# Kernel tuning notes

Measured on AMD Instinct MI355X. Metric: run time of the kernel, lower is better.

The kernel has to match this reference:

```python
import jax, jax.numpy as jnp
import numpy as np

N_NODES = 100000
N_EDGES = 3200000
F_IN = 256
D_OUT = 64
BATCH = 4096
N_FIELDS = 20


def setup_inputs() -> dict:
    key = jax.random.key(0)
    k1, k2, k3, k4 = jax.random.split(key, 4)
    features = jax.random.normal(k1, (N_NODES, F_IN), dtype=jnp.float32)
    edge_index = jax.random.randint(k2, (2, N_EDGES), 0, N_NODES, dtype=jnp.int32)
    W = jax.random.normal(k3, (F_IN, D_OUT), dtype=jnp.float32) * 0.05
    b = jnp.zeros((D_OUT,), dtype=jnp.float32)
    x = jax.random.randint(k4, (BATCH, N_FIELDS), 0, N_NODES, dtype=jnp.int32)
    return {"features": features, "edge_index": edge_index, "W": W, "b": b, "x": x}


def reference(features, edge_index, W, b, x):
    # PyG GCNConv: add self-loops, symmetric normalization, linear transform,
    # scatter-add aggregation, then final index by x.
    n = features.shape[0]
    loop = jnp.arange(n, dtype=edge_index.dtype)
    src = jnp.concatenate([edge_index[0], loop])  # [E+N]
    dst = jnp.concatenate([edge_index[1], loop])
    ones = jnp.ones(src.shape[0], dtype=features.dtype)
    deg = jax.ops.segment_sum(ones, dst, num_segments=n)  # in-degree incl. self-loop
    deg_inv_sqrt = jnp.where(deg > 0, jax.lax.rsqrt(deg), 0.0)
    norm = deg_inv_sqrt[src] * deg_inv_sqrt[dst]  # [E+N]
    xw = features @ W  # [N, D] -- transform before aggregation (fewer FLOPs)
    msg = xw[src] * norm[:, None]  # gather + scale
    out = jax.ops.segment_sum(msg, dst, num_segments=n) + b  # [N, D]
    return out[x]  # [batch, num_fields, D]
```

## Files before the change

### kernel.cpp

```cpp
#include <hip/hip_runtime.h>
#include <hip/hip_bf16.h>

#define N_NODES 100000
#define N_EDGES 3200000
#define F_IN 256
#define D_OUT 64
#define BATCH 4096
#define N_FIELDS 20
#define N_ENTRIES (BATCH * N_FIELDS)

#define NBUCKET 512
#define NPB 196
#define N_PAD (NBUCKET * NPB)
#define EPB 4096
#define NBLK ((N_EDGES + EPB - 1) / EPB)
#define BUCKET_CAP 8192
#define SCAN_B 512
#define NSB (N_PAD / SCAN_B)
#define CNT_BLKS (N_ENTRIES / 256)
#define GEMM_BLKS ((N_NODES + 63) / 64)

typedef short bf16x8 __attribute__((ext_vector_type(8)));
typedef float f32x4 __attribute__((ext_vector_type(4)));

static __device__ __forceinline__ unsigned short f2bf_bits(float x) {
    __hip_bfloat16 h = __float2bfloat16(x);
    return *reinterpret_cast<unsigned short*>(&h);
}

__global__ __launch_bounds__(256) void k_front(const uint4* __restrict__ dst4,
                                               unsigned short* __restrict__ perBlockCnt,
                                               const int* __restrict__ x,
                                               int* __restrict__ nodeEntCnt,
                                               unsigned* __restrict__ refBits,
                                               const float* __restrict__ feat,
                                               const float* __restrict__ W,
                                               float* __restrict__ yf) {
    __shared__ unsigned hist[NBUCKET];
    __shared__ unsigned short wt[64 * 264];
    int tid = threadIdx.x;

    if (blockIdx.x < NBLK) {
        hist[tid] = 0;
        hist[tid + 256] = 0;
        __syncthreads();
        int base4 = blockIdx.x * (EPB / 4);
#pragma unroll
        for (int k = 0; k < EPB / 1024; k++) {
            int e4 = base4 + k * 256 + tid;
            if (e4 < N_EDGES / 4) {
                uint4 d = dst4[e4];
                atomicAdd(&hist[d.x / NPB], 1u);
                atomicAdd(&hist[d.y / NPB], 1u);
                atomicAdd(&hist[d.z / NPB], 1u);
                atomicAdd(&hist[d.w / NPB], 1u);
            }
        }
        __syncthreads();
        perBlockCnt[(tid) * NBLK + blockIdx.x] = (unsigned short)hist[tid];
        perBlockCnt[(tid + 256) * NBLK + blockIdx.x] = (unsigned short)hist[tid + 256];
    } else if (blockIdx.x < NBLK + CNT_BLKS) {
        int ent = (blockIdx.x - NBLK) * 256 + tid;
        if (ent < N_ENTRIES) {
            int node = x[ent];
            atomicAdd(&nodeEntCnt[node], 1);
            atomicOr(&refBits[node >> 5], 1u << (node & 31));
        }
    } else {
        int gb = blockIdx.x - NBLK - CNT_BLKS;
        {
            const float4* wrow = (const float4*)(W + tid * 64);
#pragma unroll
            for (int n4 = 0; n4 < 16; n4++) {
                float4 v = wrow[n4];
                wt[(n4 * 4 + 0) * 264 + tid] = f2bf_bits(v.x);
                wt[(n4 * 4 + 1) * 264 + tid] = f2bf_bits(v.y);
                wt[(n4 * 4 + 2) * 264 + tid] = f2bf_bits(v.z);
                wt[(n4 * 4 + 3) * 264 + tid] = f2bf_bits(v.w);
            }
        }
        __syncthreads();

        int wave = tid >> 6, lane = tid & 63;
        int quad = lane >> 4, m = lane & 15;
        int rowT = gb * 64 + wave * 16;
        int row = rowT + m;
        int rowC = (row < N_NODES) ? row : (N_NODES - 1);
        const float* fb = feat + (size_t)rowC * F_IN + quad * 8;

        f32x4 acc0 = {0.f, 0.f, 0.f, 0.f};
        f32x4 acc1 = acc0, acc2 = acc0, acc3 = acc0;

#pragma unroll
        for (int kk = 0; kk < 8; kk++) {
            float4 x0 = *(const float4*)(fb + kk * 32);
            float4 x1 = *(const float4*)(fb + kk * 32 + 4);
            bf16x8 a;
            a[0] = (short)f2bf_bits(x0.x); a[1] = (short)f2bf_bits(x0.y);
            a[2] = (short)f2bf_bits(x0.z); a[3] = (short)f2bf_bits(x0.w);
            a[4] = (short)f2bf_bits(x1.x); a[5] = (short)f2bf_bits(x1.y);
            a[6] = (short)f2bf_bits(x1.z); a[7] = (short)f2bf_bits(x1.w);
            int kbase = kk * 32 + quad * 8;
            bf16x8 b0 = *(const bf16x8*)&wt[(0 * 16 + m) * 264 + kbase];
            bf16x8 b1 = *(const bf16x8*)&wt[(1 * 16 + m) * 264 + kbase];
            bf16x8 b2 = *(const bf16x8*)&wt[(2 * 16 + m) * 264 + kbase];
            bf16x8 b3 = *(const bf16x8*)&wt[(3 * 16 + m) * 264 + kbase];
            acc0 = __builtin_amdgcn_mfma_f32_16x16x32_bf16(a, b0, acc0, 0, 0, 0);
            acc1 = __builtin_amdgcn_mfma_f32_16x16x32_bf16(a, b1, acc1, 0, 0, 0);
            acc2 = __builtin_amdgcn_mfma_f32_16x16x32_bf16(a, b2, acc2, 0, 0, 0);
            acc3 = __builtin_amdgcn_mfma_f32_16x16x32_bf16(a, b3, acc3, 0, 0, 0);
        }

#pragma unroll
        for (int r = 0; r < 4; r++) {
            int rr = rowT + quad * 4 + r;
            if (rr < N_NODES) {
                size_t o = (size_t)rr * D_OUT + m;
                yf[o]      = acc0[r];
                yf[o + 16] = acc1[r];
                yf[o + 32] = acc2[r];
                yf[o + 48] = acc3[r];
            }
        }
    }
}

__global__ __launch_bounds__(512) void k_scans(const int* __restrict__ nodeEntCnt,
                                               int* __restrict__ localE,
                                               int* __restrict__ blockSumsE,
                                               unsigned short* __restrict__ perBlockCnt,
                                               int* __restrict__ bucketTot) {
    if (blockIdx.x < NSB) {
        __shared__ int sh[SCAN_B];
        int g = blockIdx.x * SCAN_B + threadIdx.x;
        int v = (g < N_PAD) ? nodeEntCnt[g] : 0;
        sh[threadIdx.x] = v;
        __syncthreads();
        for (int off = 1; off < SCAN_B; off <<= 1) {
            int t = (threadIdx.x >= off) ? sh[threadIdx.x - off] : 0;
            __syncthreads();
            sh[threadIdx.x] += t;
            __syncthreads();
        }
        int incl = sh[threadIdx.x];
        if (g < N_PAD) localE[g] = incl - v;
        if (threadIdx.x == SCAN_B - 1) blockSumsE[blockIdx.x] = incl;
    } else {
        int gw = ((blockIdx.x - NSB) * 512 + threadIdx.x) >> 6;
        int lane = threadIdx.x & 63;
        if (gw >= NBUCKET) return;
        unsigned running = 0;
        for (int c = 0; c < (NBLK + 63) / 64; c++) {
            int blk = c * 64 + lane;
            int idx = gw * NBLK + blk;
            unsigned v = (blk < NBLK) ? perBlockCnt[idx] : 0;
            unsigned orig = v;
#pragma unroll
            for (int d = 1; d < 64; d <<= 1) {
                unsigned t = __shfl_up(v, d, 64);
                if (lane >= d) v += t;
            }
            if (blk < NBLK) perBlockCnt[idx] = (unsigned short)(running + v - orig);
            running += __shfl(v, 63, 64);
        }
        if (lane == 0) bucketTot[gw] = (int)running;
    }
}

__global__ __launch_bounds__(512) void k_base2(const int* __restrict__ bucketTot,
                                               int* __restrict__ bucketBase,
                                               const int* __restrict__ blockSumsE,
                                               int* __restrict__ blockBaseE) {
    __shared__ int sh[512];
    int tid = threadIdx.x;
    if (blockIdx.x == 0) {
        int v = bucketTot[tid];
        sh[tid] = v;
        __syncthreads();
        for (int off = 1; off < 512; off <<= 1) {
            int t = (tid >= off) ? sh[tid - off] : 0;
            __syncthreads();
            sh[tid] += t;
            __syncthreads();
        }
        bucketBase[tid] = sh[tid] - v;
        if (tid == NBUCKET - 1) bucketBase[NBUCKET] = sh[NBUCKET - 1];
    } else {
        int v = (tid < NSB) ? blockSumsE[tid] : 0;
        sh[tid] = v;
        __syncthreads();
        for (int off = 1; off < 512; off <<= 1) {
            int t = (tid >= off) ? sh[tid - off] : 0;
            __syncthreads();
            sh[tid] += t;
            __syncthreads();
        }
        if (tid < NSB) blockBaseE[tid] = sh[tid] - v;
    }
}

__global__ __launch_bounds__(256) void k_scatters(const uint4* __restrict__ src4,
                                                  const uint4* __restrict__ dst4,
                                                  const int* __restrict__ bucketBase,
                                                  const unsigned short* __restrict__ perBlockCnt,
                                                  unsigned* __restrict__ bucketData,
                                                  const int* __restrict__ x,
                                                  int* __restrict__ localE,
                                                  const int* __restrict__ blockBaseE,
                                                  int* __restrict__ entGrouped) {
    if (blockIdx.x < NBLK) {
        __shared__ unsigned slotBase[NBUCKET];
        slotBase[threadIdx.x] = (unsigned)bucketBase[threadIdx.x] +
                                (unsigned)perBlockCnt[threadIdx.x * NBLK + blockIdx.x];
        slotBase[threadIdx.x + 256] = (unsigned)bucketBase[threadIdx.x + 256] +
                                      (unsigned)perBlockCnt[(threadIdx.x + 256) * NBLK + blockIdx.x];
        __syncthreads();
        int base4 = blockIdx.x * (EPB / 4);
#pragma unroll
        for (int k = 0; k < EPB / 1024; k++) {
            int e4 = base4 + k * 256 + threadIdx.x;
            if (e4 < N_EDGES / 4) {
                uint4 s = src4[e4];
                uint4 d = dst4[e4];
                unsigned ss[4] = {s.x, s.y, s.z, s.w};
                unsigned dd[4] = {d.x, d.y, d.z, d.w};
#pragma unroll
                for (int j = 0; j < 4; j++) {
                    unsigned b = dd[j] / NPB;
                    unsigned ld = dd[j] - b * NPB;
                    unsigned slot = atomicAdd(&slotBase[b], 1u);
                    bucketData[slot] = ss[j] | (ld << 17);
                }
            }
        }
    } else {
        int ent = (blockIdx.x - NBLK) * 256 + threadIdx.x;
        if (ent < N_ENTRIES) {
            int node = x[ent];
            int posL = atomicAdd(&localE[node], 1);
            entGrouped[blockBaseE[node >> 9] + posL] = ent;
        }
    }
}

__global__ __launch_bounds__(256) void k_bucket_csr(unsigned* __restrict__ bucketData,
                                                    const int* __restrict__ bucketBase,
                                                    const unsigned* __restrict__ refBits,
                                                    int* __restrict__ rowStart,
                                                    unsigned short* __restrict__ deg,
                                                    const float* __restrict__ yf,
                                                    unsigned short* __restrict__ y) {
    __shared__ unsigned srcsorted[BUCKET_CAP];
    __shared__ unsigned nodeCount[NPB];
    __shared__ unsigned sscan[256];
    __shared__ unsigned cursor[NPB];
    __shared__ unsigned char refF[NPB];

    int b = blockIdx.x;
    int base = bucketBase[b];
    int cnt = bucketBase[b + 1] - base;
    if (cnt > BUCKET_CAP) cnt = BUCKET_CAP;
    int tid = threadIdx.x;

    for (int j = tid; j < NPB; j += 256) nodeCount[j] = 0;
    __syncthreads();

    for (int i = tid; i < cnt; i += 256) {
        unsigned w = bucketData[base + i];
        atomicAdd(&nodeCount[w >> 17], 1u);
    }
    __syncthreads();

    int firstNode = b * NPB;
    unsigned refCnt = 0;
    if (tid < NPB) {
        int node = firstNode + tid;
        unsigned isRef = (refBits[node >> 5] >> (node & 31)) & 1u;
        refF[tid] = (unsigned char)isRef;
        refCnt = isRef ? nodeCount[tid] : 0;
        deg[node] = (unsigned short)nodeCount[tid];
    }
    sscan[tid] = refCnt;
    __syncthreads();
    for (int off = 1; off < 256; off <<= 1) {
        unsigned t = (tid >= off) ? sscan[tid - off] : 0;
        __syncthreads();
        sscan[tid] += t;
        __syncthreads();
    }

    if (tid < NPB) {
        unsigned excl = sscan[tid] - refCnt;
        rowStart[firstNode + tid] = base + (int)excl;
        cursor[tid] = excl;
    }
    __syncthreads();

    for (int i = tid; i < cnt; i += 256) {
        unsigned w = bucketData[base + i];
        unsigned ld = w >> 17;
        if (refF[ld]) {
            unsigned slot = atomicAdd(&cursor[ld], 1u);
            srcsorted[slot] = w & 0x1FFFFu;
        }
    }
    __syncthreads();

    int refTotal = (int)sscan[255];
    for (int i = tid; i < refTotal; i += 256)
        bucketData[base + i] = srcsorted[i];

    for (int idx = tid; idx < NPB * 16; idx += 256) {
        int j = idx >> 4;
        int node = firstNode + j;
        if (node < N_NODES) {
            float ds = rsqrtf((float)nodeCount[j] + 1.0f);
            float4 v = ((const float4*)(yf + (size_t)node * D_OUT))[idx & 15];
            uint2 pw;
            pw.x = (unsigned)f2bf_bits(v.x * ds) | ((unsigned)f2bf_bits(v.y * ds) << 16);
            pw.y = (unsigned)f2bf_bits(v.z * ds) | ((unsigned)f2bf_bits(v.w * ds) << 16);
            ((uint2*)(y + (size_t)node * D_OUT))[idx & 15] = pw;
        }
    }
}

static __device__ __forceinline__ void acc4(f32x4& a, uint2 v, float msk) {
    a[0] += msk * __uint_as_float(v.x << 16);
    a[1] += msk * __uint_as_float(v.x & 0xffff0000u);
    a[2] += msk * __uint_as_float(v.y << 16);
    a[3] += msk * __uint_as_float(v.y & 0xffff0000u);
}

__global__ __launch_bounds__(256) void k_agg(const int* __restrict__ entGrouped,
                                             const int* __restrict__ localE,
                                             const int* __restrict__ blockBaseE,
                                             const int* __restrict__ rowStart,
                                             const unsigned short* __restrict__ deg,
                                             const unsigned* __restrict__ sortedSrc,
                                             const unsigned short* __restrict__ y,
                                             const float* __restrict__ b,
                                             float* __restrict__ out) {
    int g = blockIdx.x * blockDim.x + threadIdx.x;
    int i = g >> 6, lane = g & 63;
    if (i >= N_PAD) return;
    int gEnd = blockBaseE[i >> 9] + localE[i];
    int gStart = (i == 0) ? 0 : (blockBaseE[(i - 1) >> 9] + localE[i - 1]);
    int cntEnt = gEnd - gStart;
    if (cntEnt <= 0) return;

    int grp = lane >> 4;
    int m = lane & 15;
    int start = rowStart[i];
    int cnt = deg[i];
    float disI = rsqrtf((float)(cnt + 1));

    uint2 sv = *(const uint2*)(y + ((unsigned)i << 6) + (m << 2));

    f32x4 a0 = {0.f, 0.f, 0.f, 0.f};
    f32x4 a1 = a0, a2 = a0, a3 = a0;

    for (int e = 0; e < cnt; e += 32) {
        int e0 = e + grp,      e1 = e + 4 + grp,  e2 = e + 8 + grp,  e3 = e + 12 + grp;
        int e4 = e + 16 + grp, e5 = e + 20 + grp, e6 = e + 24 + grp, e7 = e + 28 + grp;
        unsigned r0 = (e0 < cnt) ? sortedSrc[start + e0] : (unsigned)i;
        unsigned r1 = (e1 < cnt) ? sortedSrc[start + e1] : (unsigned)i;
        unsigned r2 = (e2 < cnt) ? sortedSrc[start + e2] : (unsigned)i;
        unsigned r3 = (e3 < cnt) ? sortedSrc[start + e3] : (unsigned)i;
        unsigned r4 = (e4 < cnt) ? sortedSrc[start + e4] : (unsigned)i;
        unsigned r5 = (e5 < cnt) ? sortedSrc[start + e5] : (unsigned)i;
        unsigned r6 = (e6 < cnt) ? sortedSrc[start + e6] : (unsigned)i;
        unsigned r7 = (e7 < cnt) ? sortedSrc[start + e7] : (unsigned)i;
        uint2 v0 = *(const uint2*)(y + (r0 << 6) + (m << 2));
        uint2 v1 = *(const uint2*)(y + (r1 << 6) + (m << 2));
        uint2 v2 = *(const uint2*)(y + (r2 << 6) + (m << 2));
        uint2 v3 = *(const uint2*)(y + (r3 << 6) + (m << 2));
        uint2 v4 = *(const uint2*)(y + (r4 << 6) + (m << 2));
        uint2 v5 = *(const uint2*)(y + (r5 << 6) + (m << 2));
        uint2 v6 = *(const uint2*)(y + (r6 << 6) + (m << 2));
        uint2 v7 = *(const uint2*)(y + (r7 << 6) + (m << 2));
        acc4(a0, v0, (e0 < cnt) ? 1.f : 0.f);
        acc4(a1, v1, (e1 < cnt) ? 1.f : 0.f);
        acc4(a2, v2, (e2 < cnt) ? 1.f : 0.f);
        acc4(a3, v3, (e3 < cnt) ? 1.f : 0.f);
        acc4(a0, v4, (e4 < cnt) ? 1.f : 0.f);
        acc4(a1, v5, (e5 < cnt) ? 1.f : 0.f);
        acc4(a2, v6, (e6 < cnt) ? 1.f : 0.f);
        acc4(a3, v7, (e7 < cnt) ? 1.f : 0.f);
    }

    f32x4 s;
#pragma unroll
    for (int c = 0; c < 4; c++) s[c] = (a0[c] + a1[c]) + (a2[c] + a3[c]);
#pragma unroll
    for (int c = 0; c < 4; c++) {
        s[c] += __shfl_xor(s[c], 16, 64);
        s[c] += __shfl_xor(s[c], 32, 64);
    }

    float4 b4 = *(const float4*)(b + (m << 2));
    float4 val;
    val.x = disI * (s[0] + __uint_as_float(sv.x << 16)) + b4.x;
    val.y = disI * (s[1] + __uint_as_float(sv.x & 0xffff0000u)) + b4.y;
    val.z = disI * (s[2] + __uint_as_float(sv.y << 16)) + b4.z;
    val.w = disI * (s[3] + __uint_as_float(sv.y & 0xffff0000u)) + b4.w;

    for (int j = grp; j < cntEnt; j += 4) {
        int ent = entGrouped[gStart + j];
        *(float4*)(out + (size_t)ent * D_OUT + (m << 2)) = val;
    }
}

extern "C" void kernel_launch(void* const* d_in, const int* in_sizes, int n_in,
                              void* d_out, int out_size, void* d_ws, size_t ws_size,
                              hipStream_t stream) {
    const float* feat     = (const float*)d_in[0];
    const int* edge_index = (const int*)d_in[1];
    const float* W        = (const float*)d_in[2];
    const float* bsrc     = (const float*)d_in[3];
    const int* x          = (const int*)d_in[4];
    float* out            = (float*)d_out;

    const uint4* src4 = (const uint4*)edge_index;
    const uint4* dst4 = (const uint4*)(edge_index + N_EDGES);

    char* ws = (char*)d_ws;
    size_t off = 0;
    auto alloc = [&](size_t bytes) {
        size_t o = off;
        off = (off + bytes + 255) & ~(size_t)255;
        return o;
    };
    size_t pcBytes = (size_t)NBUCKET * NBLK * 2;
    size_t rsBytes = (pcBytes > (size_t)N_PAD * 4) ? pcBytes : (size_t)N_PAD * 4;
    int* bucketBase = (int*)(ws + alloc((size_t)(NBUCKET + 1) * 4));
    int* bucketTot  = (int*)(ws + alloc((size_t)NBUCKET * 4));
    size_t ecOff = alloc((size_t)N_PAD * 4);
    int* nodeEntCnt = (int*)(ws + ecOff);
    int* entGrouped = (int*)(ws + ecOff);
    unsigned* refBits = (unsigned*)(ws + alloc((size_t)(N_PAD / 8)));
    size_t rsOff = alloc(rsBytes);
    unsigned short* perBlockCnt = (unsigned short*)(ws + rsOff);
    int* rowStart   = (int*)(ws + rsOff);
    unsigned short* deg = (unsigned short*)(ws + alloc((size_t)N_PAD * 2));
    int* localE     = (int*)(ws + alloc((size_t)N_PAD * 4));
    int* blockSumsE = (int*)(ws + alloc((size_t)NSB * 4));
    int* blockBaseE = (int*)(ws + alloc((size_t)NSB * 4));
    unsigned* bucketData = (unsigned*)(ws + alloc((size_t)N_EDGES * 4));
    unsigned short* y = (unsigned short*)(ws + alloc((size_t)N_NODES * D_OUT * 2));
    float* yf       = (float*)(ws + alloc((size_t)N_NODES * D_OUT * 4));
    (void)ws_size; (void)in_sizes; (void)n_in; (void)out_size;

    const int T = 256;
    (void)hipMemsetAsync(nodeEntCnt, 0, (size_t)N_PAD * 4, stream);
    (void)hipMemsetAsync(refBits, 0, (size_t)(N_PAD / 8), stream);
    k_front<<<NBLK + CNT_BLKS + GEMM_BLKS, T, 0, stream>>>(dst4, perBlockCnt, x, nodeEntCnt,
                                                           refBits, feat, W, yf);
    k_scans<<<NSB + 64, 512, 0, stream>>>(nodeEntCnt, localE, blockSumsE, perBlockCnt, bucketTot);
    k_base2<<<2, 512, 0, stream>>>(bucketTot, bucketBase, blockSumsE, blockBaseE);
    k_scatters<<<NBLK + CNT_BLKS, T, 0, stream>>>(src4, dst4, bucketBase, perBlockCnt, bucketData,
                                                  x, localE, blockBaseE, entGrouped);
    k_bucket_csr<<<NBUCKET, T, 0, stream>>>(bucketData, bucketBase, refBits, rowStart, deg, yf, y);
    k_agg<<<((size_t)N_PAD * 64 + T - 1) / T, T, 0, stream>>>(
        entGrouped, localE, blockBaseE, rowStart, deg, bucketData, y, bsrc, out);
}
```

Baseline: 314.5 us.

## Replace scan-based bucket partition with atomic cursors and broadcast per-node results

The edge bucketing now reserves space per bucket with global atomic cursors into fixed-capacity bucket regions, all inside the front kernel. This removes the per-block histogram scans, the base-offset kernel and the separate scatter pass. The entry grouping by node is also dropped: aggregation writes per-node results for referenced nodes to a buffer, and a new broadcast kernel gathers those rows into the output by x. This cuts three launches and several passes over the data, in exchange for nondeterministic edge order within a bucket, silent truncation if a bucket exceeds its capacity, and an extra intermediate write and read.

```diff
diff --git a/kernel.cpp b/kernel.cpp
--- a/kernel.cpp
+++ b/kernel.cpp
@@ -15,10 +15,9 @@
 #define EPB 4096
 #define NBLK ((N_EDGES + EPB - 1) / EPB)
 #define BUCKET_CAP 8192
-#define SCAN_B 512
-#define NSB (N_PAD / SCAN_B)
 #define CNT_BLKS (N_ENTRIES / 256)
 #define GEMM_BLKS ((N_NODES + 63) / 64)
+#define BCAST_BLKS (N_ENTRIES / 16)
 
 typedef short bf16x8 __attribute__((ext_vector_type(8)));
 typedef float f32x4 __attribute__((ext_vector_type(4)));
@@ -28,21 +27,22 @@
     return *reinterpret_cast<unsigned short*>(&h);
 }
 
-__global__ __launch_bounds__(256) void k_front(const uint4* __restrict__ dst4,
-                                               unsigned short* __restrict__ perBlockCnt,
+__global__ __launch_bounds__(256) void k_front(const uint4* __restrict__ src4,
+                                               const uint4* __restrict__ dst4,
+                                               unsigned* __restrict__ gCursor,
+                                               unsigned* __restrict__ bucketData,
                                                const int* __restrict__ x,
-                                               int* __restrict__ nodeEntCnt,
                                                unsigned* __restrict__ refBits,
                                                const float* __restrict__ feat,
                                                const float* __restrict__ W,
                                                float* __restrict__ yf) {
-    __shared__ unsigned hist[NBUCKET];
+    __shared__ unsigned cur[NBUCKET];
     __shared__ unsigned short wt[64 * 264];
     int tid = threadIdx.x;
 
     if (blockIdx.x < NBLK) {
-        hist[tid] = 0;
-        hist[tid + 256] = 0;
+        cur[tid] = 0;
+        cur[tid + 256] = 0;
         __syncthreads();
         int base4 = blockIdx.x * (EPB / 4);
 #pragma unroll
@@ -50,20 +50,42 @@
             int e4 = base4 + k * 256 + tid;
             if (e4 < N_EDGES / 4) {
                 uint4 d = dst4[e4];
-                atomicAdd(&hist[d.x / NPB], 1u);
-                atomicAdd(&hist[d.y / NPB], 1u);
-                atomicAdd(&hist[d.z / NPB], 1u);
-                atomicAdd(&hist[d.w / NPB], 1u);
+                atomicAdd(&cur[d.x / NPB], 1u);
+                atomicAdd(&cur[d.y / NPB], 1u);
+                atomicAdd(&cur[d.z / NPB], 1u);
+                atomicAdd(&cur[d.w / NPB], 1u);
             }
         }
         __syncthreads();
-        perBlockCnt[(tid) * NBLK + blockIdx.x] = (unsigned short)hist[tid];
-        perBlockCnt[(tid + 256) * NBLK + blockIdx.x] = (unsigned short)hist[tid + 256];
+        unsigned c0 = cur[tid], c1 = cur[tid + 256];
+        unsigned b0 = c0 ? atomicAdd(&gCursor[tid], c0) : 0u;
+        unsigned b1 = c1 ? atomicAdd(&gCursor[tid + 256], c1) : 0u;
+        __syncthreads();
+        cur[tid] = (unsigned)tid * BUCKET_CAP + b0;
+        cur[tid + 256] = (unsigned)(tid + 256) * BUCKET_CAP + b1;
+        __syncthreads();
+#pragma unroll
+        for (int k = 0; k < EPB / 1024; k++) {
+            int e4 = base4 + k * 256 + tid;
+            if (e4 < N_EDGES / 4) {
+                uint4 s = src4[e4];
+                uint4 d = dst4[e4];
+                unsigned ss[4] = {s.x, s.y, s.z, s.w};
+                unsigned dd[4] = {d.x, d.y, d.z, d.w};
+#pragma unroll
+                for (int j = 0; j < 4; j++) {
+                    unsigned b = dd[j] / NPB;
+                    unsigned ld = dd[j] - b * NPB;
+                    unsigned slot = atomicAdd(&cur[b], 1u);
+                    if (slot < (b + 1u) * BUCKET_CAP)
+                        bucketData[slot] = ss[j] | (ld << 17);
+                }
+            }
+        }
     } else if (blockIdx.x < NBLK + CNT_BLKS) {
         int ent = (blockIdx.x - NBLK) * 256 + tid;
         if (ent < N_ENTRIES) {
             int node = x[ent];
-            atomicAdd(&nodeEntCnt[node], 1);
             atomicOr(&refBits[node >> 5], 1u << (node & 31));
         }
     } else {
@@ -125,126 +147,8 @@
     }
 }
 
-__global__ __launch_bounds__(512) void k_scans(const int* __restrict__ nodeEntCnt,
-                                               int* __restrict__ localE,
-                                               int* __restrict__ blockSumsE,
-                                               unsigned short* __restrict__ perBlockCnt,
-                                               int* __restrict__ bucketTot) {
-    if (blockIdx.x < NSB) {
-        __shared__ int sh[SCAN_B];
-        int g = blockIdx.x * SCAN_B + threadIdx.x;
-        int v = (g < N_PAD) ? nodeEntCnt[g] : 0;
-        sh[threadIdx.x] = v;
-        __syncthreads();
-        for (int off = 1; off < SCAN_B; off <<= 1) {
-            int t = (threadIdx.x >= off) ? sh[threadIdx.x - off] : 0;
-            __syncthreads();
-            sh[threadIdx.x] += t;
-            __syncthreads();
-        }
-        int incl = sh[threadIdx.x];
-        if (g < N_PAD) localE[g] = incl - v;
-        if (threadIdx.x == SCAN_B - 1) blockSumsE[blockIdx.x] = incl;
-    } else {
-        int gw = ((blockIdx.x - NSB) * 512 + threadIdx.x) >> 6;
-        int lane = threadIdx.x & 63;
-        if (gw >= NBUCKET) return;
-        unsigned running = 0;
-        for (int c = 0; c < (NBLK + 63) / 64; c++) {
-            int blk = c * 64 + lane;
-            int idx = gw * NBLK + blk;
-            unsigned v = (blk < NBLK) ? perBlockCnt[idx] : 0;
-            unsigned orig = v;
-#pragma unroll
-            for (int d = 1; d < 64; d <<= 1) {
-                unsigned t = __shfl_up(v, d, 64);
-                if (lane >= d) v += t;
-            }
-            if (blk < NBLK) perBlockCnt[idx] = (unsigned short)(running + v - orig);
-            running += __shfl(v, 63, 64);
-        }
-        if (lane == 0) bucketTot[gw] = (int)running;
-    }
-}
-
-__global__ __launch_bounds__(512) void k_base2(const int* __restrict__ bucketTot,
-                                               int* __restrict__ bucketBase,
-                                               const int* __restrict__ blockSumsE,
-                                               int* __restrict__ blockBaseE) {
-    __shared__ int sh[512];
-    int tid = threadIdx.x;
-    if (blockIdx.x == 0) {
-        int v = bucketTot[tid];
-        sh[tid] = v;
-        __syncthreads();
-        for (int off = 1; off < 512; off <<= 1) {
-            int t = (tid >= off) ? sh[tid - off] : 0;
-            __syncthreads();
-            sh[tid] += t;
-            __syncthreads();
-        }
-        bucketBase[tid] = sh[tid] - v;
-        if (tid == NBUCKET - 1) bucketBase[NBUCKET] = sh[NBUCKET - 1];
-    } else {
-        int v = (tid < NSB) ? blockSumsE[tid] : 0;
-        sh[tid] = v;
-        __syncthreads();
-        for (int off = 1; off < 512; off <<= 1) {
-            int t = (tid >= off) ? sh[tid - off] : 0;
-            __syncthreads();
-            sh[tid] += t;
-            __syncthreads();
-        }
-        if (tid < NSB) blockBaseE[tid] = sh[tid] - v;
-    }
-}
-
-__global__ __launch_bounds__(256) void k_scatters(const uint4* __restrict__ src4,
-                                                  const uint4* __restrict__ dst4,
-                                                  const int* __restrict__ bucketBase,
-                                                  const unsigned short* __restrict__ perBlockCnt,
-                                                  unsigned* __restrict__ bucketData,
-                                                  const int* __restrict__ x,
-                                                  int* __restrict__ localE,
-                                                  const int* __restrict__ blockBaseE,
-                                                  int* __restrict__ entGrouped) {
-    if (blockIdx.x < NBLK) {
-        __shared__ unsigned slotBase[NBUCKET];
-        slotBase[threadIdx.x] = (unsigned)bucketBase[threadIdx.x] +
-                                (unsigned)perBlockCnt[threadIdx.x * NBLK + blockIdx.x];
-        slotBase[threadIdx.x + 256] = (unsigned)bucketBase[threadIdx.x + 256] +
-                                      (unsigned)perBlockCnt[(threadIdx.x + 256) * NBLK + blockIdx.x];
-        __syncthreads();
-        int base4 = blockIdx.x * (EPB / 4);
-#pragma unroll
-        for (int k = 0; k < EPB / 1024; k++) {
-            int e4 = base4 + k * 256 + threadIdx.x;
-            if (e4 < N_EDGES / 4) {
-                uint4 s = src4[e4];
-                uint4 d = dst4[e4];
-                unsigned ss[4] = {s.x, s.y, s.z, s.w};
-                unsigned dd[4] = {d.x, d.y, d.z, d.w};
-#pragma unroll
-                for (int j = 0; j < 4; j++) {
-                    unsigned b = dd[j] / NPB;
-                    unsigned ld = dd[j] - b * NPB;
-                    unsigned slot = atomicAdd(&slotBase[b], 1u);
-                    bucketData[slot] = ss[j] | (ld << 17);
-                }
-            }
-        }
-    } else {
-        int ent = (blockIdx.x - NBLK) * 256 + threadIdx.x;
-        if (ent < N_ENTRIES) {
-            int node = x[ent];
-            int posL = atomicAdd(&localE[node], 1);
-            entGrouped[blockBaseE[node >> 9] + posL] = ent;
-        }
-    }
-}
-
 __global__ __launch_bounds__(256) void k_bucket_csr(unsigned* __restrict__ bucketData,
-                                                    const int* __restrict__ bucketBase,
+                                                    const unsigned* __restrict__ gCursor,
                                                     const unsigned* __restrict__ refBits,
                                                     int* __restrict__ rowStart,
                                                     unsigned short* __restrict__ deg,
@@ -257,8 +161,8 @@
     __shared__ unsigned char refF[NPB];
 
     int b = blockIdx.x;
-    int base = bucketBase[b];
-    int cnt = bucketBase[b + 1] - base;
+    int base = b * BUCKET_CAP;
+    int cnt = (int)gCursor[b];
     if (cnt > BUCKET_CAP) cnt = BUCKET_CAP;
     int tid = threadIdx.x;
 
@@ -331,22 +235,17 @@
     a[3] += msk * __uint_as_float(v.y & 0xffff0000u);
 }
 
-__global__ __launch_bounds__(256) void k_agg(const int* __restrict__ entGrouped,
-                                             const int* __restrict__ localE,
-                                             const int* __restrict__ blockBaseE,
+__global__ __launch_bounds__(256) void k_agg(const unsigned* __restrict__ refBits,
                                              const int* __restrict__ rowStart,
                                              const unsigned short* __restrict__ deg,
                                              const unsigned* __restrict__ sortedSrc,
                                              const unsigned short* __restrict__ y,
                                              const float* __restrict__ b,
-                                             float* __restrict__ out) {
+                                             float* __restrict__ valN) {
     int g = blockIdx.x * blockDim.x + threadIdx.x;
     int i = g >> 6, lane = g & 63;
     if (i >= N_PAD) return;
-    int gEnd = blockBaseE[i >> 9] + localE[i];
-    int gStart = (i == 0) ? 0 : (blockBaseE[(i - 1) >> 9] + localE[i - 1]);
-    int cntEnt = gEnd - gStart;
-    if (cntEnt <= 0) return;
+    if (!((refBits[i >> 5] >> (i & 31)) & 1u)) return;
 
     int grp = lane >> 4;
     int m = lane & 15;
@@ -397,17 +296,26 @@
         s[c] += __shfl_xor(s[c], 32, 64);
     }
 
-    float4 b4 = *(const float4*)(b + (m << 2));
-    float4 val;
-    val.x = disI * (s[0] + __uint_as_float(sv.x << 16)) + b4.x;
-    val.y = disI * (s[1] + __uint_as_float(sv.x & 0xffff0000u)) + b4.y;
-    val.z = disI * (s[2] + __uint_as_float(sv.y << 16)) + b4.z;
-    val.w = disI * (s[3] + __uint_as_float(sv.y & 0xffff0000u)) + b4.w;
-
-    for (int j = grp; j < cntEnt; j += 4) {
-        int ent = entGrouped[gStart + j];
-        *(float4*)(out + (size_t)ent * D_OUT + (m << 2)) = val;
-    }
+    if (grp == 0) {
+        float4 b4 = *(const float4*)(b + (m << 2));
+        float4 val;
+        val.x = disI * (s[0] + __uint_as_float(sv.x << 16)) + b4.x;
+        val.y = disI * (s[1] + __uint_as_float(sv.x & 0xffff0000u)) + b4.y;
+        val.z = disI * (s[2] + __uint_as_float(sv.y << 16)) + b4.z;
+        val.w = disI * (s[3] + __uint_as_float(sv.y & 0xffff0000u)) + b4.w;
+        *(float4*)(valN + (size_t)i * D_OUT + (m << 2)) = val;
+    }
+}
+
+__global__ __launch_bounds__(256) void k_bcast(const int* __restrict__ x,
+                                               const float* __restrict__ valN,
+                                               float* __restrict__ out) {
+    int tid = threadIdx.x;
+    int ent = blockIdx.x * 16 + (tid >> 4);
+    int q = tid & 15;
+    int node = x[ent];
+    float4 v = ((const float4*)(valN + (size_t)node * D_OUT))[q];
+    ((float4*)(out + (size_t)ent * D_OUT))[q] = v;
 }
 
 extern "C" void kernel_launch(void* const* d_in, const int* in_sizes, int n_in,
@@ -430,36 +338,23 @@
         off = (off + bytes + 255) & ~(size_t)255;
         return o;
     };
-    size_t pcBytes = (size_t)NBUCKET * NBLK * 2;
-    size_t rsBytes = (pcBytes > (size_t)N_PAD * 4) ? pcBytes : (size_t)N_PAD * 4;
-    int* bucketBase = (int*)(ws + alloc((size_t)(NBUCKET + 1) * 4));
-    int* bucketTot  = (int*)(ws + alloc((size_t)NBUCKET * 4));
-    size_t ecOff = alloc((size_t)N_PAD * 4);
-    int* nodeEntCnt = (int*)(ws + ecOff);
-    int* entGrouped = (int*)(ws + ecOff);
-    unsigned* refBits = (unsigned*)(ws + alloc((size_t)(N_PAD / 8)));
-    size_t rsOff = alloc(rsBytes);
-    unsigned short* perBlockCnt = (unsigned short*)(ws + rsOff);
-    int* rowStart   = (int*)(ws + rsOff);
+    unsigned* gCursor   = (unsigned*)(ws + alloc((size_t)NBUCKET * 4));
+    unsigned* refBits   = (unsigned*)(ws + alloc((size_t)(N_PAD / 8)));
+    int* rowStart       = (int*)(ws + alloc((size_t)N_PAD * 4));
     unsigned short* deg = (unsigned short*)(ws + alloc((size_t)N_PAD * 2));
-    int* localE     = (int*)(ws + alloc((size_t)N_PAD * 4));
-    int* blockSumsE = (int*)(ws + alloc((size_t)NSB * 4));
-    int* blockBaseE = (int*)(ws + alloc((size_t)NSB * 4));
-    unsigned* bucketData = (unsigned*)(ws + alloc((size_t)N_EDGES * 4));
-    unsigned short* y = (unsigned short*)(ws + alloc((size_t)N_NODES * D_OUT * 2));
-    float* yf       = (float*)(ws + alloc((size_t)N_NODES * D_OUT * 4));
+    unsigned* bucketData = (unsigned*)(ws + alloc((size_t)NBUCKET * BUCKET_CAP * 4));
+    unsigned short* y   = (unsigned short*)(ws + alloc((size_t)N_NODES * D_OUT * 2));
+    float* yf           = (float*)(ws + alloc((size_t)N_NODES * D_OUT * 4));
+    float* valN         = (float*)(ws + alloc((size_t)N_PAD * D_OUT * 4));
     (void)ws_size; (void)in_sizes; (void)n_in; (void)out_size;
 
     const int T = 256;
-    (void)hipMemsetAsync(nodeEntCnt, 0, (size_t)N_PAD * 4, stream);
+    (void)hipMemsetAsync(gCursor, 0, (size_t)NBUCKET * 4, stream);
     (void)hipMemsetAsync(refBits, 0, (size_t)(N_PAD / 8), stream);
-    k_front<<<NBLK + CNT_BLKS + GEMM_BLKS, T, 0, stream>>>(dst4, perBlockCnt, x, nodeEntCnt,
-                                                           refBits, feat, W, yf);
-    k_scans<<<NSB + 64, 512, 0, stream>>>(nodeEntCnt, localE, blockSumsE, perBlockCnt, bucketTot);
-    k_base2<<<2, 512, 0, stream>>>(bucketTot, bucketBase, blockSumsE, blockBaseE);
-    k_scatters<<<NBLK + CNT_BLKS, T, 0, stream>>>(src4, dst4, bucketBase, perBlockCnt, bucketData,
-                                                  x, localE, blockBaseE, entGrouped);
-    k_bucket_csr<<<NBUCKET, T, 0, stream>>>(bucketData, bucketBase, refBits, rowStart, deg, yf, y);
+    k_front<<<NBLK + CNT_BLKS + GEMM_BLKS, T, 0, stream>>>(src4, dst4, gCursor, bucketData,
+                                                           x, refBits, feat, W, yf);
+    k_bucket_csr<<<NBUCKET, T, 0, stream>>>(bucketData, gCursor, refBits, rowStart, deg, yf, y);
     k_agg<<<((size_t)N_PAD * 64 + T - 1) / T, T, 0, stream>>>(
-        entGrouped, localE, blockBaseE, rowStart, deg, bucketData, y, bsrc, out);
-}
+        refBits, rowStart, deg, bucketData, y, bsrc, valN);
+    k_bcast<<<BCAST_BLKS, T, 0, stream>>>(x, valN, out);
+}
```

After: 319.8 us. No clear change (+1.7%).
